# Kernel tuning notes

Measured on AMD Instinct MI355X. Metric: run time of the kernel, lower is better.

The kernel has to match this reference:

```python
import jax, jax.numpy as jnp
import numpy as np

N, F, HID, HEADS, C, E = 4096, 128, 128, 8, 64, 131072
HEAD_DIM = F // HEADS


def gcn_conv(x, row, col, W, b):
    # PyG GCNConv: add self-loops, symmetric normalization, then scatter-add of X@W.
    n = x.shape[0]
    loops = jnp.arange(n)
    r = jnp.concatenate([row, loops])
    c = jnp.concatenate([col, loops])
    deg = jax.ops.segment_sum(jnp.ones_like(c, x.dtype), c, num_segments=n)
    dinv = jnp.where(deg > 0, jax.lax.rsqrt(deg), 0.0)
    norm = dinv[r] * dinv[c]                      # [E+N]
    h = x @ W                                      # [n, out]
    msg = h[r] * norm[:, None]                     # gather + scale
    return jax.ops.segment_sum(msg, c, num_segments=n) + b


def mha(x, in_w, in_b, out_w, out_b):
    # torch nn.MultiheadAttention, unbatched (L, E) self-attention
    n, e = x.shape
    qkv = x @ in_w.T + in_b                        # [n, 3E]
    q, k, v = jnp.split(qkv, 3, axis=-1)
    q = q.reshape(n, HEADS, HEAD_DIM).transpose(1, 0, 2)
    k = k.reshape(n, HEADS, HEAD_DIM).transpose(1, 0, 2)
    v = v.reshape(n, HEADS, HEAD_DIM).transpose(1, 0, 2)
    scores = jnp.einsum('hnd,hmd->hnm', q, k) / jnp.sqrt(jnp.asarray(HEAD_DIM, x.dtype))
    attn = jax.nn.softmax(scores, axis=-1)
    o = jnp.einsum('hnm,hmd->hnd', attn, v).transpose(1, 0, 2).reshape(n, e)
    return o @ out_w.T + out_b


def setup_inputs() -> dict:
    key = jax.random.key(0)
    ks = jax.random.split(key, 14)

    def lin(k, shape, fan_in):
        return jax.random.uniform(k, shape, jnp.float32, -1.0, 1.0) / np.sqrt(fan_in)

    return {
        'x': jax.random.normal(ks[0], (N, F), jnp.float32),
        'edge_index': jax.random.randint(ks[1], (2, E), 0, N),
        'W1': lin(ks[2], (F, HID), F), 'b1': lin(ks[3], (HID,), F),
        'W2': lin(ks[4], (HID, HID), HID), 'b2': lin(ks[5], (HID,), HID),
        'W3': lin(ks[6], (HID, C), HID), 'b3': lin(ks[7], (C,), HID),
        'in_proj_w': lin(ks[8], (3 * F, F), F), 'in_proj_b': jnp.zeros((3 * F,), jnp.float32),
        'out_proj_w': lin(ks[9], (F, F), F), 'out_proj_b': jnp.zeros((F,), jnp.float32),
        'proj_w': lin(ks[10], (F, C), F), 'proj_b': lin(ks[11], (C,), F),
    }


def reference(x, edge_index, W1, b1, W2, b2, W3, b3,
              in_proj_w, in_proj_b, out_proj_w, out_proj_b, proj_w, proj_b):
    row, col = edge_index[0], edge_index[1]
    h = jax.nn.relu(gcn_conv(x, row, col, W1, b1))
    h = jax.nn.relu(gcn_conv(h, row, col, W2, b2))
    x_gnn = h @ W3 + b3                           # [N, C]
    x_tf = mha(x, in_proj_w, in_proj_b, out_proj_w, out_proj_b)
    x_proj = x_tf @ proj_w + proj_b               # [N, C]
    return jax.nn.relu(x_gnn + x_proj)
```

## Files before the change

### kernel.cpp

```cpp
#include <hip/hip_runtime.h>
#include <math.h>

#define N_NODES 4096
#define F_DIM   128
#define E_EDGES 131072
#define NHEADS  8
#define HD      16
#define C_OUT   64

__global__ void deg_count(const int* __restrict__ col, int* __restrict__ deg) {
  int e = blockIdx.x * blockDim.x + threadIdx.x;
  if (e < E_EDGES) atomicAdd(&deg[col[e]], 1);
}

__global__ void dinv_kernel(const int* __restrict__ deg, float* __restrict__ dinv) {
  int i = blockIdx.x * blockDim.x + threadIdx.x;
  if (i < N_NODES) dinv[i] = rsqrtf((float)(deg[i] + 1));
}

__global__ void scan_kernel(const int* __restrict__ deg, int* __restrict__ offs) {
  __shared__ int part[1024];
  int t = threadIdx.x;
  int v0 = deg[t*4+0], v1 = deg[t*4+1], v2 = deg[t*4+2], v3 = deg[t*4+3];
  int s = v0 + v1 + v2 + v3;
  part[t] = s;
  __syncthreads();
  for (int off = 1; off < 1024; off <<= 1) {
    int x = (t >= off) ? part[t - off] : 0;
    __syncthreads();
    part[t] += x;
    __syncthreads();
  }
  int excl = part[t] - s;
  offs[t*4+0] = excl; excl += v0;
  offs[t*4+1] = excl; excl += v1;
  offs[t*4+2] = excl; excl += v2;
  offs[t*4+3] = excl; excl += v3;
  if (t == 1023) offs[4096] = excl;
}

__global__ void fill_csr(const int* __restrict__ row, const int* __restrict__ col,
                         const int* __restrict__ offs, int* __restrict__ cursor,
                         int* __restrict__ src) {
  int e = blockIdx.x * blockDim.x + threadIdx.x;
  if (e < E_EDGES) {
    int c = col[e];
    int p = atomicAdd(&cursor[c], 1);
    src[offs[c] + p] = row[e];
  }
}

__global__ void gcn_agg(const float* __restrict__ t, const float* __restrict__ dinv,
                        const int* __restrict__ offs, const int* __restrict__ src,
                        const float* __restrict__ bias, float* __restrict__ out) {
  int c = blockIdx.x;
  int f = threadIdx.x;
  float dc = dinv[c];
  float acc = t[c * F_DIM + f] * dc;
  int e = offs[c], end = offs[c + 1];
  for (; e + 4 <= end; e += 4) {
    int r0 = src[e], r1 = src[e+1], r2 = src[e+2], r3 = src[e+3];
    float w0 = dinv[r0], w1 = dinv[r1], w2 = dinv[r2], w3 = dinv[r3];
    float v0 = t[r0*F_DIM + f], v1 = t[r1*F_DIM + f];
    float v2 = t[r2*F_DIM + f], v3 = t[r3*F_DIM + f];
    acc += v0*w0 + v1*w1 + v2*w2 + v3*w3;
  }
  for (; e < end; ++e) { int r = src[e]; acc += t[r*F_DIM + f] * dinv[r]; }
  float res = acc * dc + bias[f];
  out[c * F_DIM + f] = fmaxf(res, 0.f);
}

template<int TM, bool NT, bool BIAS, bool RELU, bool EXTRA>
__global__ __launch_bounds__(256) void gemm2(const float* __restrict__ A,
                                             const float* __restrict__ B,
                                             const float* __restrict__ bias,
                                             const float* __restrict__ extra,
                                             float* __restrict__ C,
                                             int ldb, int ldc) {
  constexpr int K = 128, BK = 32, TN = 64;
  constexpr int RM = TM * TN / 1024;
  constexpr int LDA = 36;
  constexpr int LDB = TN + 4;
  __shared__ float As[BK * LDA];
  __shared__ float Bs[BK * LDB];
  const int tid = threadIdx.x;
  const int tx = tid & 15;
  const int ty = tid >> 4;
  const int row0 = blockIdx.x * TM;
  const int jg0  = blockIdx.y * TN;

  float acc[RM][4];
  #pragma unroll
  for (int r = 0; r < RM; ++r) { acc[r][0]=0.f; acc[r][1]=0.f; acc[r][2]=0.f; acc[r][3]=0.f; }

  for (int kc = 0; kc < K; kc += BK) {
    __syncthreads();
    {
      constexpr int NL = TM * BK / 4;
      for (int idx = tid; idx < NL; idx += 256) {
        int m  = idx >> 3;
        int k4 = idx & 7;
        const float4 g = *(const float4*)&A[(row0 + m) * K + kc + k4 * 4];
        As[(k4*4+0)*LDA + m] = g.x;
        As[(k4*4+1)*LDA + m] = g.y;
        As[(k4*4+2)*LDA + m] = g.z;
        As[(k4*4+3)*LDA + m] = g.w;
      }
    }
    if constexpr (NT) {
      constexpr int NL = TN * 8;
      for (int idx = tid; idx < NL; idx += 256) {
        int n  = idx >> 3;
        int k4 = idx & 7;
        const float4 g = *(const float4*)&B[(jg0 + n) * K + kc + k4 * 4];
        Bs[(k4*4+0)*LDB + n] = g.x;
        Bs[(k4*4+1)*LDB + n] = g.y;
        Bs[(k4*4+2)*LDB + n] = g.z;
        Bs[(k4*4+3)*LDB + n] = g.w;
      }
    } else {
      constexpr int NL = BK * TN / 4;
      for (int idx = tid; idx < NL; idx += 256) {
        int k  = idx >> 4;
        int n4 = idx & 15;
        *(float4*)&Bs[k * LDB + n4 * 4] =
            *(const float4*)&B[(kc + k) * ldb + jg0 + n4 * 4];
      }
    }
    __syncthreads();
    #pragma unroll
    for (int k = 0; k < BK; ++k) {
      const float4 bv = *(const float4*)&Bs[k * LDB + tx * 4];
      #pragma unroll
      for (int r = 0; r < RM; ++r) {
        const float a = As[k * LDA + ty * RM + r];
        acc[r][0] = fmaf(a, bv.x, acc[r][0]);
        acc[r][1] = fmaf(a, bv.y, acc[r][1]);
        acc[r][2] = fmaf(a, bv.z, acc[r][2]);
        acc[r][3] = fmaf(a, bv.w, acc[r][3]);
      }
    }
  }

  #pragma unroll
  for (int r = 0; r < RM; ++r) {
    const int gr = row0 + ty * RM + r;
    const int gc = jg0 + tx * 4;
    float4 v = make_float4(acc[r][0], acc[r][1], acc[r][2], acc[r][3]);
    if constexpr (BIAS) {
      const float4 bb = *(const float4*)&bias[gc];
      v.x += bb.x; v.y += bb.y; v.z += bb.z; v.w += bb.w;
    }
    if constexpr (EXTRA) {
      const float4 e = *(const float4*)&extra[gr * ldc + gc];
      v.x += e.x; v.y += e.y; v.z += e.z; v.w += e.w;
    }
    if constexpr (RELU) {
      v.x = fmaxf(v.x, 0.f); v.y = fmaxf(v.y, 0.f);
      v.z = fmaxf(v.z, 0.f); v.w = fmaxf(v.w, 0.f);
    }
    *(float4*)&C[gr * ldc + gc] = v;
  }
}

__global__ __launch_bounds__(256) void attn_kernel(const float* __restrict__ qkv,
                                                   float* __restrict__ o) {
  constexpr int TQ = 64, TK = 512;
  __shared__ float Ks[TK * HD];
  __shared__ float Vs[TK * HD];
  const int h    = blockIdx.y;
  const int rl   = threadIdx.x >> 2;
  const int sub  = threadIdx.x & 3;
  const int rowg = blockIdx.x * TQ + rl;

  const float4* qp = (const float4*)&qkv[rowg * 384 + h * HD];
  float4 q0 = qp[0], q1 = qp[1], q2 = qp[2], q3 = qp[3];
  q0.x*=0.25f; q0.y*=0.25f; q0.z*=0.25f; q0.w*=0.25f;
  q1.x*=0.25f; q1.y*=0.25f; q1.z*=0.25f; q1.w*=0.25f;
  q2.x*=0.25f; q2.y*=0.25f; q2.z*=0.25f; q2.w*=0.25f;
  q3.x*=0.25f; q3.y*=0.25f; q3.z*=0.25f; q3.w*=0.25f;

  float m = -INFINITY, l = 0.f;
  float oa[HD];
  #pragma unroll
  for (int d = 0; d < HD; ++d) oa[d] = 0.f;

  for (int kt = 0; kt < N_NODES; kt += TK) {
    __syncthreads();
    for (int fi = threadIdx.x; fi < TK * HD / 4; fi += 256) {
      int r = fi >> 2, c4 = fi & 3;
      ((float4*)Ks)[fi] = *(const float4*)&qkv[(kt + r) * 384 + 128 + h * HD + c4 * 4];
      ((float4*)Vs)[fi] = *(const float4*)&qkv[(kt + r) * 384 + 256 + h * HD + c4 * 4];
    }
    __syncthreads();

    for (int j0 = 0; j0 < TK; j0 += 32) {
      float s[8];
      #pragma unroll
      for (int i = 0; i < 8; ++i) {
        const float4* kp = (const float4*)&Ks[(j0 + 4*i + sub) * HD];
        const float4 k0 = kp[0], k1 = kp[1], k2 = kp[2], k3 = kp[3];
        float p0 = fmaf(q0.x,k0.x, fmaf(q0.y,k0.y, fmaf(q0.z,k0.z, q0.w*k0.w)));
        float p1 = fmaf(q1.x,k1.x, fmaf(q1.y,k1.y, fmaf(q1.z,k1.z, q1.w*k1.w)));
        float p2 = fmaf(q2.x,k2.x, fmaf(q2.y,k2.y, fmaf(q2.z,k2.z, q2.w*k2.w)));
        float p3 = fmaf(q3.x,k3.x, fmaf(q3.y,k3.y, fmaf(q3.z,k3.z, q3.w*k3.w)));
        s[i] = (p0 + p1) + (p2 + p3);
      }
      float bm = fmaxf(fmaxf(fmaxf(s[0],s[1]), fmaxf(s[2],s[3])),
                       fmaxf(fmaxf(s[4],s[5]), fmaxf(s[6],s[7])));
      float mnew = fmaxf(m, bm);
      float cor = __expf(m - mnew);
      float p[8];
      #pragma unroll
      for (int i = 0; i < 8; ++i) p[i] = __expf(s[i] - mnew);
      float ps = ((p[0]+p[1]) + (p[2]+p[3])) + ((p[4]+p[5]) + (p[6]+p[7]));
      l = fmaf(l, cor, ps);
      m = mnew;
      #pragma unroll
      for (int d = 0; d < HD; ++d) oa[d] *= cor;
      #pragma unroll
      for (int i = 0; i < 8; ++i) {
        const float4* vp = (const float4*)&Vs[(j0 + 4*i + sub) * HD];
        const float4 v0 = vp[0], v1 = vp[1], v2 = vp[2], v3 = vp[3];
        oa[0]  = fmaf(p[i], v0.x, oa[0]);  oa[1]  = fmaf(p[i], v0.y, oa[1]);
        oa[2]  = fmaf(p[i], v0.z, oa[2]);  oa[3]  = fmaf(p[i], v0.w, oa[3]);
        oa[4]  = fmaf(p[i], v1.x, oa[4]);  oa[5]  = fmaf(p[i], v1.y, oa[5]);
        oa[6]  = fmaf(p[i], v1.z, oa[6]);  oa[7]  = fmaf(p[i], v1.w, oa[7]);
        oa[8]  = fmaf(p[i], v2.x, oa[8]);  oa[9]  = fmaf(p[i], v2.y, oa[9]);
        oa[10] = fmaf(p[i], v2.z, oa[10]); oa[11] = fmaf(p[i], v2.w, oa[11]);
        oa[12] = fmaf(p[i], v3.x, oa[12]); oa[13] = fmaf(p[i], v3.y, oa[13]);
        oa[14] = fmaf(p[i], v3.z, oa[14]); oa[15] = fmaf(p[i], v3.w, oa[15]);
      }
    }
  }
  __syncthreads();
  Vs[rl*4 + sub]       = m;
  Vs[256 + rl*4 + sub] = l;
  #pragma unroll
  for (int d = 0; d < HD; ++d) Ks[(rl*4 + sub) * HD + d] = oa[d];
  __syncthreads();
  float m0 = Vs[rl*4+0], m1 = Vs[rl*4+1], m2 = Vs[rl*4+2], m3 = Vs[rl*4+3];
  float M  = fmaxf(fmaxf(m0, m1), fmaxf(m2, m3));
  float w0 = __expf(m0 - M), w1 = __expf(m1 - M), w2 = __expf(m2 - M), w3 = __expf(m3 - M);
  float L  = Vs[256+rl*4+0]*w0 + Vs[256+rl*4+1]*w1 + Vs[256+rl*4+2]*w2 + Vs[256+rl*4+3]*w3;
  float invL = 1.f / L;
  const float* kb = &Ks[rl * 4 * HD];
  int d0 = sub * 4;
  float4 r;
  r.x = (kb[0*HD+d0+0]*w0 + kb[1*HD+d0+0]*w1 + kb[2*HD+d0+0]*w2 + kb[3*HD+d0+0]*w3) * invL;
  r.y = (kb[0*HD+d0+1]*w0 + kb[1*HD+d0+1]*w1 + kb[2*HD+d0+1]*w2 + kb[3*HD+d0+1]*w3) * invL;
  r.z = (kb[0*HD+d0+2]*w0 + kb[1*HD+d0+2]*w1 + kb[2*HD+d0+2]*w2 + kb[3*HD+d0+2]*w3) * invL;
  r.w = (kb[0*HD+d0+3]*w0 + kb[1*HD+d0+3]*w1 + kb[2*HD+d0+3]*w2 + kb[3*HD+d0+3]*w3) * invL;
  *(float4*)&o[rowg * F_DIM + h * HD + d0] = r;
}

extern "C" void kernel_launch(void* const* d_in, const int* in_sizes, int n_in,
                              void* d_out, int out_size, void* d_ws, size_t ws_size,
                              hipStream_t stream) {
  const float* x   = (const float*)d_in[0];
  const int*   ei  = (const int*)  d_in[1];
  const float* W1  = (const float*)d_in[2];
  const float* b1  = (const float*)d_in[3];
  const float* W2  = (const float*)d_in[4];
  const float* b2  = (const float*)d_in[5];
  const float* W3  = (const float*)d_in[6];
  const float* b3  = (const float*)d_in[7];
  const float* ipw = (const float*)d_in[8];
  const float* ipb = (const float*)d_in[9];
  const float* opw = (const float*)d_in[10];
  const float* opb = (const float*)d_in[11];
  const float* pw  = (const float*)d_in[12];
  const float* pb  = (const float*)d_in[13];
  float* out = (float*)d_out;

  int*   deg    = (int*)d_ws;
  int*   cursor = deg + 4096;
  int*   offs   = cursor + 4096;
  int*   csrc   = offs + 4100;
  float* dinv   = (float*)(csrc + E_EDGES);
  float* bufA   = dinv + 4096;
  float* bufB   = bufA + 524288;
  float* qkv    = bufB + 524288;
  float* obuf   = qkv + 1572864;

  const int* rowp = ei;
  const int* colp = ei + E_EDGES;

  hipMemsetAsync(deg, 0, 8192 * sizeof(int), stream);
  deg_count<<<E_EDGES / 256, 256, 0, stream>>>(colp, deg);
  dinv_kernel<<<N_NODES / 256, 256, 0, stream>>>(deg, dinv);
  scan_kernel<<<1, 1024, 0, stream>>>(deg, offs);
  fill_csr<<<E_EDGES / 256, 256, 0, stream>>>(rowp, colp, offs, cursor, csrc);

  gemm2<32, false, false, false, false><<<dim3(128, 2), 256, 0, stream>>>(
      x, W1, nullptr, nullptr, bufA, 128, 128);
  gcn_agg<<<N_NODES, 128, 0, stream>>>(bufA, dinv, offs, csrc, b1, bufB);
  gemm2<32, false, false, false, false><<<dim3(128, 2), 256, 0, stream>>>(
      bufB, W2, nullptr, nullptr, bufA, 128, 128);
  gcn_agg<<<N_NODES, 128, 0, stream>>>(bufA, dinv, offs, csrc, b2, bufB);
  gemm2<16, false, true, false, false><<<dim3(256, 1), 256, 0, stream>>>(
      bufB, W3, b3, nullptr, bufA, 64, C_OUT);

  gemm2<32, true, true, false, false><<<dim3(128, 6), 256, 0, stream>>>(
      x, ipw, ipb, nullptr, qkv, 128, 384);
  attn_kernel<<<dim3(64, NHEADS), 256, 0, stream>>>(qkv, obuf);
  gemm2<32, true, true, false, false><<<dim3(128, 2), 256, 0, stream>>>(
      obuf, opw, opb, nullptr, bufB, 128, 128);
  gemm2<16, false, true, true, true><<<dim3(256, 1), 256, 0, stream>>>(
      bufB, pw, pb, bufA, out, 64, C_OUT);
}
```

Baseline: 382.1 us.

## Fuse dinv into scan, vectorize GCN aggregation, retile attention, merge final GEMMs

Several changes land together. dinv is computed inside the scan kernel, removing one launch. GCN aggregation now gives each node a 32-lane group that loads float4 values, with 8 nodes per block. Attention threads each cover 4 query rows against 16 key slices, for more register reuse per shared-memory load, with a 16-way merge at the end and launch bounds set for 2 blocks. The W3 GEMM and the projection GEMM become one dual-pass GEMM that sums both products with both biases, dropping a kernel and an intermediate write and read. The costs are higher register pressure in attention and a larger final merge step.

Result: faster. 337.2 us (-11.8%).

```diff
diff --git a/kernel.cpp b/kernel.cpp
--- a/kernel.cpp
+++ b/kernel.cpp
@@ -13,15 +13,15 @@
   if (e < E_EDGES) atomicAdd(&deg[col[e]], 1);
 }
 
-__global__ void dinv_kernel(const int* __restrict__ deg, float* __restrict__ dinv) {
-  int i = blockIdx.x * blockDim.x + threadIdx.x;
-  if (i < N_NODES) dinv[i] = rsqrtf((float)(deg[i] + 1));
-}
-
-__global__ void scan_kernel(const int* __restrict__ deg, int* __restrict__ offs) {
+__global__ void scan_kernel(const int* __restrict__ deg, int* __restrict__ offs,
+                            float* __restrict__ dinv) {
   __shared__ int part[1024];
   int t = threadIdx.x;
   int v0 = deg[t*4+0], v1 = deg[t*4+1], v2 = deg[t*4+2], v3 = deg[t*4+3];
+  dinv[t*4+0] = rsqrtf((float)(v0 + 1));
+  dinv[t*4+1] = rsqrtf((float)(v1 + 1));
+  dinv[t*4+2] = rsqrtf((float)(v2 + 1));
+  dinv[t*4+3] = rsqrtf((float)(v3 + 1));
   int s = v0 + v1 + v2 + v3;
   part[t] = s;
   __syncthreads();
@@ -50,31 +50,53 @@
   }
 }
 
-__global__ void gcn_agg(const float* __restrict__ t, const float* __restrict__ dinv,
-                        const int* __restrict__ offs, const int* __restrict__ src,
-                        const float* __restrict__ bias, float* __restrict__ out) {
-  int c = blockIdx.x;
-  int f = threadIdx.x;
-  float dc = dinv[c];
-  float acc = t[c * F_DIM + f] * dc;
-  int e = offs[c], end = offs[c + 1];
-  for (; e + 4 <= end; e += 4) {
-    int r0 = src[e], r1 = src[e+1], r2 = src[e+2], r3 = src[e+3];
-    float w0 = dinv[r0], w1 = dinv[r1], w2 = dinv[r2], w3 = dinv[r3];
-    float v0 = t[r0*F_DIM + f], v1 = t[r1*F_DIM + f];
-    float v2 = t[r2*F_DIM + f], v3 = t[r3*F_DIM + f];
-    acc += v0*w0 + v1*w1 + v2*w2 + v3*w3;
-  }
-  for (; e < end; ++e) { int r = src[e]; acc += t[r*F_DIM + f] * dinv[r]; }
-  float res = acc * dc + bias[f];
-  out[c * F_DIM + f] = fmaxf(res, 0.f);
-}
-
-template<int TM, bool NT, bool BIAS, bool RELU, bool EXTRA>
+__global__ __launch_bounds__(256) void gcn_agg(const float* __restrict__ t,
+                                               const float* __restrict__ dinv,
+                                               const int* __restrict__ offs,
+                                               const int* __restrict__ src,
+                                               const float* __restrict__ bias,
+                                               float* __restrict__ out) {
+  const int node = blockIdx.x * 8 + (threadIdx.x >> 5);
+  const int lane = threadIdx.x & 31;
+  const float dc = dinv[node];
+  float4 a0 = *(const float4*)&t[node * F_DIM + lane * 4];
+  a0.x *= dc; a0.y *= dc; a0.z *= dc; a0.w *= dc;
+  float4 a1 = make_float4(0.f, 0.f, 0.f, 0.f);
+  int e = offs[node], end = offs[node + 1];
+  for (; e + 2 <= end; e += 2) {
+    int r0 = src[e], r1 = src[e + 1];
+    float w0 = dinv[r0], w1 = dinv[r1];
+    const float4 v0 = *(const float4*)&t[r0 * F_DIM + lane * 4];
+    const float4 v1 = *(const float4*)&t[r1 * F_DIM + lane * 4];
+    a0.x = fmaf(w0, v0.x, a0.x); a0.y = fmaf(w0, v0.y, a0.y);
+    a0.z = fmaf(w0, v0.z, a0.z); a0.w = fmaf(w0, v0.w, a0.w);
+    a1.x = fmaf(w1, v1.x, a1.x); a1.y = fmaf(w1, v1.y, a1.y);
+    a1.z = fmaf(w1, v1.z, a1.z); a1.w = fmaf(w1, v1.w, a1.w);
+  }
+  if (e < end) {
+    int r0 = src[e];
+    float w0 = dinv[r0];
+    const float4 v0 = *(const float4*)&t[r0 * F_DIM + lane * 4];
+    a0.x = fmaf(w0, v0.x, a0.x); a0.y = fmaf(w0, v0.y, a0.y);
+    a0.z = fmaf(w0, v0.z, a0.z); a0.w = fmaf(w0, v0.w, a0.w);
+  }
+  a0.x += a1.x; a0.y += a1.y; a0.z += a1.z; a0.w += a1.w;
+  const float4 bb = *(const float4*)&bias[lane * 4];
+  float4 r;
+  r.x = fmaxf(fmaf(a0.x, dc, bb.x), 0.f);
+  r.y = fmaxf(fmaf(a0.y, dc, bb.y), 0.f);
+  r.z = fmaxf(fmaf(a0.z, dc, bb.z), 0.f);
+  r.w = fmaxf(fmaf(a0.w, dc, bb.w), 0.f);
+  *(float4*)&out[node * F_DIM + lane * 4] = r;
+}
+
+template<int TM, bool NT, bool BIAS, bool RELU, bool DUAL>
 __global__ __launch_bounds__(256) void gemm2(const float* __restrict__ A,
                                              const float* __restrict__ B,
                                              const float* __restrict__ bias,
-                                             const float* __restrict__ extra,
+                                             const float* __restrict__ A2,
+                                             const float* __restrict__ B2,
+                                             const float* __restrict__ bias2,
                                              float* __restrict__ C,
                                              int ldb, int ldc) {
   constexpr int K = 128, BK = 32, TN = 64;
@@ -93,51 +115,55 @@
   #pragma unroll
   for (int r = 0; r < RM; ++r) { acc[r][0]=0.f; acc[r][1]=0.f; acc[r][2]=0.f; acc[r][3]=0.f; }
 
-  for (int kc = 0; kc < K; kc += BK) {
-    __syncthreads();
-    {
-      constexpr int NL = TM * BK / 4;
-      for (int idx = tid; idx < NL; idx += 256) {
-        int m  = idx >> 3;
-        int k4 = idx & 7;
-        const float4 g = *(const float4*)&A[(row0 + m) * K + kc + k4 * 4];
-        As[(k4*4+0)*LDA + m] = g.x;
-        As[(k4*4+1)*LDA + m] = g.y;
-        As[(k4*4+2)*LDA + m] = g.z;
-        As[(k4*4+3)*LDA + m] = g.w;
-      }
-    }
-    if constexpr (NT) {
-      constexpr int NL = TN * 8;
-      for (int idx = tid; idx < NL; idx += 256) {
-        int n  = idx >> 3;
-        int k4 = idx & 7;
-        const float4 g = *(const float4*)&B[(jg0 + n) * K + kc + k4 * 4];
-        Bs[(k4*4+0)*LDB + n] = g.x;
-        Bs[(k4*4+1)*LDB + n] = g.y;
-        Bs[(k4*4+2)*LDB + n] = g.z;
-        Bs[(k4*4+3)*LDB + n] = g.w;
-      }
-    } else {
-      constexpr int NL = BK * TN / 4;
-      for (int idx = tid; idx < NL; idx += 256) {
-        int k  = idx >> 4;
-        int n4 = idx & 15;
-        *(float4*)&Bs[k * LDB + n4 * 4] =
-            *(const float4*)&B[(kc + k) * ldb + jg0 + n4 * 4];
-      }
-    }
-    __syncthreads();
-    #pragma unroll
-    for (int k = 0; k < BK; ++k) {
-      const float4 bv = *(const float4*)&Bs[k * LDB + tx * 4];
+  for (int pass = 0; pass < (DUAL ? 2 : 1); ++pass) {
+    const float* Ap = (DUAL && pass) ? A2 : A;
+    const float* Bp = (DUAL && pass) ? B2 : B;
+    for (int kc = 0; kc < K; kc += BK) {
+      __syncthreads();
+      {
+        constexpr int NL = TM * BK / 4;
+        for (int idx = tid; idx < NL; idx += 256) {
+          int m  = idx >> 3;
+          int k4 = idx & 7;
+          const float4 g = *(const float4*)&Ap[(row0 + m) * K + kc + k4 * 4];
+          As[(k4*4+0)*LDA + m] = g.x;
+          As[(k4*4+1)*LDA + m] = g.y;
+          As[(k4*4+2)*LDA + m] = g.z;
+          As[(k4*4+3)*LDA + m] = g.w;
+        }
+      }
+      if constexpr (NT) {
+        constexpr int NL = TN * 8;
+        for (int idx = tid; idx < NL; idx += 256) {
+          int n  = idx >> 3;
+          int k4 = idx & 7;
+          const float4 g = *(const float4*)&Bp[(jg0 + n) * K + kc + k4 * 4];
+          Bs[(k4*4+0)*LDB + n] = g.x;
+          Bs[(k4*4+1)*LDB + n] = g.y;
+          Bs[(k4*4+2)*LDB + n] = g.z;
+          Bs[(k4*4+3)*LDB + n] = g.w;
+        }
+      } else {
+        constexpr int NL = BK * TN / 4;
+        for (int idx = tid; idx < NL; idx += 256) {
+          int k  = idx >> 4;
+          int n4 = idx & 15;
+          *(float4*)&Bs[k * LDB + n4 * 4] =
+              *(const float4*)&Bp[(kc + k) * ldb + jg0 + n4 * 4];
+        }
+      }
+      __syncthreads();
       #pragma unroll
-      for (int r = 0; r < RM; ++r) {
-        const float a = As[k * LDA + ty * RM + r];
-        acc[r][0] = fmaf(a, bv.x, acc[r][0]);
-        acc[r][1] = fmaf(a, bv.y, acc[r][1]);
-        acc[r][2] = fmaf(a, bv.z, acc[r][2]);
-        acc[r][3] = fmaf(a, bv.w, acc[r][3]);
+      for (int k = 0; k < BK; ++k) {
+        const float4 bv = *(const float4*)&Bs[k * LDB + tx * 4];
+        #pragma unroll
+        for (int r = 0; r < RM; ++r) {
+          const float a = As[k * LDA + ty * RM + r];
+          acc[r][0] = fmaf(a, bv.x, acc[r][0]);
+          acc[r][1] = fmaf(a, bv.y, acc[r][1]);
+          acc[r][2] = fmaf(a, bv.z, acc[r][2]);
+          acc[r][3] = fmaf(a, bv.w, acc[r][3]);
+        }
       }
     }
   }
@@ -151,9 +177,9 @@
       const float4 bb = *(const float4*)&bias[gc];
       v.x += bb.x; v.y += bb.y; v.z += bb.z; v.w += bb.w;
     }
-    if constexpr (EXTRA) {
-      const float4 e = *(const float4*)&extra[gr * ldc + gc];
-      v.x += e.x; v.y += e.y; v.z += e.z; v.w += e.w;
+    if constexpr (DUAL) {
+      const float4 bb = *(const float4*)&bias2[gc];
+      v.x += bb.x; v.y += bb.y; v.z += bb.z; v.w += bb.w;
     }
     if constexpr (RELU) {
       v.x = fmaxf(v.x, 0.f); v.y = fmaxf(v.y, 0.f);
@@ -163,27 +189,37 @@
   }
 }
 
-__global__ __launch_bounds__(256) void attn_kernel(const float* __restrict__ qkv,
-                                                   float* __restrict__ o) {
+__global__ __launch_bounds__(256, 2) void attn_kernel(const float* __restrict__ qkv,
+                                                      float* __restrict__ o) {
   constexpr int TQ = 64, TK = 512;
-  __shared__ float Ks[TK * HD];
-  __shared__ float Vs[TK * HD];
-  const int h    = blockIdx.y;
-  const int rl   = threadIdx.x >> 2;
-  const int sub  = threadIdx.x & 3;
-  const int rowg = blockIdx.x * TQ + rl;
-
-  const float4* qp = (const float4*)&qkv[rowg * 384 + h * HD];
-  float4 q0 = qp[0], q1 = qp[1], q2 = qp[2], q3 = qp[3];
-  q0.x*=0.25f; q0.y*=0.25f; q0.z*=0.25f; q0.w*=0.25f;
-  q1.x*=0.25f; q1.y*=0.25f; q1.z*=0.25f; q1.w*=0.25f;
-  q2.x*=0.25f; q2.y*=0.25f; q2.z*=0.25f; q2.w*=0.25f;
-  q3.x*=0.25f; q3.y*=0.25f; q3.z*=0.25f; q3.w*=0.25f;
-
-  float m = -INFINITY, l = 0.f;
-  float oa[HD];
-  #pragma unroll
-  for (int d = 0; d < HD; ++d) oa[d] = 0.f;
+  __shared__ float smem[2 * TK * HD + 2 * TQ * 16];
+  float* Ks = smem;
+  float* Vs = smem + TK * HD;
+  float* mbuf = smem + 2 * TK * HD;
+  float* lbuf = mbuf + TQ * 16;
+  const int h   = blockIdx.y;
+  const int rg  = threadIdx.x >> 4;
+  const int sub = threadIdx.x & 15;
+  const int row0 = blockIdx.x * TQ + rg * 4;
+
+  float4 q[4][4];
+  #pragma unroll
+  for (int r = 0; r < 4; ++r) {
+    const float4* qp = (const float4*)&qkv[(row0 + r) * 384 + h * HD];
+    #pragma unroll
+    for (int c = 0; c < 4; ++c) {
+      float4 v = qp[c];
+      v.x *= 0.25f; v.y *= 0.25f; v.z *= 0.25f; v.w *= 0.25f;
+      q[r][c] = v;
+    }
+  }
+  float m[4] = {-INFINITY, -INFINITY, -INFINITY, -INFINITY};
+  float l[4] = {0.f, 0.f, 0.f, 0.f};
+  float4 oa[4][4];
+  #pragma unroll
+  for (int r = 0; r < 4; ++r)
+    #pragma unroll
+    for (int c = 0; c < 4; ++c) oa[r][c] = make_float4(0.f, 0.f, 0.f, 0.f);
 
   for (int kt = 0; kt < N_NODES; kt += TK) {
     __syncthreads();
@@ -194,64 +230,85 @@
     }
     __syncthreads();
 
-    for (int j0 = 0; j0 < TK; j0 += 32) {
-      float s[8];
+    for (int j0 = 0; j0 < TK; j0 += 64) {
+      float s[4][4];
       #pragma unroll
-      for (int i = 0; i < 8; ++i) {
-        const float4* kp = (const float4*)&Ks[(j0 + 4*i + sub) * HD];
+      for (int kk = 0; kk < 4; ++kk) {
+        const float4* kp = (const float4*)&Ks[(j0 + kk * 16 + sub) * HD];
         const float4 k0 = kp[0], k1 = kp[1], k2 = kp[2], k3 = kp[3];
-        float p0 = fmaf(q0.x,k0.x, fmaf(q0.y,k0.y, fmaf(q0.z,k0.z, q0.w*k0.w)));
-        float p1 = fmaf(q1.x,k1.x, fmaf(q1.y,k1.y, fmaf(q1.z,k1.z, q1.w*k1.w)));
-        float p2 = fmaf(q2.x,k2.x, fmaf(q2.y,k2.y, fmaf(q2.z,k2.z, q2.w*k2.w)));
-        float p3 = fmaf(q3.x,k3.x, fmaf(q3.y,k3.y, fmaf(q3.z,k3.z, q3.w*k3.w)));
-        s[i] = (p0 + p1) + (p2 + p3);
-      }
-      float bm = fmaxf(fmaxf(fmaxf(s[0],s[1]), fmaxf(s[2],s[3])),
-                       fmaxf(fmaxf(s[4],s[5]), fmaxf(s[6],s[7])));
-      float mnew = fmaxf(m, bm);
-      float cor = __expf(m - mnew);
-      float p[8];
+        #pragma unroll
+        for (int r = 0; r < 4; ++r) {
+          float p0 = fmaf(q[r][0].x,k0.x, fmaf(q[r][0].y,k0.y, fmaf(q[r][0].z,k0.z, q[r][0].w*k0.w)));
+          float p1 = fmaf(q[r][1].x,k1.x, fmaf(q[r][1].y,k1.y, fmaf(q[r][1].z,k1.z, q[r][1].w*k1.w)));
+          float p2 = fmaf(q[r][2].x,k2.x, fmaf(q[r][2].y,k2.y, fmaf(q[r][2].z,k2.z, q[r][2].w*k2.w)));
+          float p3 = fmaf(q[r][3].x,k3.x, fmaf(q[r][3].y,k3.y, fmaf(q[r][3].z,k3.z, q[r][3].w*k3.w)));
+          s[r][kk] = (p0 + p1) + (p2 + p3);
+        }
+      }
       #pragma unroll
-      for (int i = 0; i < 8; ++i) p[i] = __expf(s[i] - mnew);
-      float ps = ((p[0]+p[1]) + (p[2]+p[3])) + ((p[4]+p[5]) + (p[6]+p[7]));
-      l = fmaf(l, cor, ps);
-      m = mnew;
+      for (int r = 0; r < 4; ++r) {
+        float bm = fmaxf(fmaxf(s[r][0], s[r][1]), fmaxf(s[r][2], s[r][3]));
+        float mn = fmaxf(m[r], bm);
+        float cor = __expf(m[r] - mn);
+        m[r] = mn;
+        s[r][0] = __expf(s[r][0] - mn);
+        s[r][1] = __expf(s[r][1] - mn);
+        s[r][2] = __expf(s[r][2] - mn);
+        s[r][3] = __expf(s[r][3] - mn);
+        l[r] = fmaf(l[r], cor, (s[r][0] + s[r][1]) + (s[r][2] + s[r][3]));
+        #pragma unroll
+        for (int c = 0; c < 4; ++c) {
+          oa[r][c].x *= cor; oa[r][c].y *= cor; oa[r][c].z *= cor; oa[r][c].w *= cor;
+        }
+      }
       #pragma unroll
-      for (int d = 0; d < HD; ++d) oa[d] *= cor;
-      #pragma unroll
-      for (int i = 0; i < 8; ++i) {
-        const float4* vp = (const float4*)&Vs[(j0 + 4*i + sub) * HD];
+      for (int kk = 0; kk < 4; ++kk) {
+        const float4* vp = (const float4*)&Vs[(j0 + kk * 16 + sub) * HD];
         const float4 v0 = vp[0], v1 = vp[1], v2 = vp[2], v3 = vp[3];
-        oa[0]  = fmaf(p[i], v0.x, oa[0]);  oa[1]  = fmaf(p[i], v0.y, oa[1]);
-        oa[2]  = fmaf(p[i], v0.z, oa[2]);  oa[3]  = fmaf(p[i], v0.w, oa[3]);
-        oa[4]  = fmaf(p[i], v1.x, oa[4]);  oa[5]  = fmaf(p[i], v1.y, oa[5]);
-        oa[6]  = fmaf(p[i], v1.z, oa[6]);  oa[7]  = fmaf(p[i], v1.w, oa[7]);
-        oa[8]  = fmaf(p[i], v2.x, oa[8]);  oa[9]  = fmaf(p[i], v2.y, oa[9]);
-        oa[10] = fmaf(p[i], v2.z, oa[10]); oa[11] = fmaf(p[i], v2.w, oa[11]);
-        oa[12] = fmaf(p[i], v3.x, oa[12]); oa[13] = fmaf(p[i], v3.y, oa[13]);
-        oa[14] = fmaf(p[i], v3.z, oa[14]); oa[15] = fmaf(p[i], v3.w, oa[15]);
+        #pragma unroll
+        for (int r = 0; r < 4; ++r) {
+          const float p = s[r][kk];
+          oa[r][0].x = fmaf(p, v0.x, oa[r][0].x); oa[r][0].y = fmaf(p, v0.y, oa[r][0].y);
+          oa[r][0].z = fmaf(p, v0.z, oa[r][0].z); oa[r][0].w = fmaf(p, v0.w, oa[r][0].w);
+          oa[r][1].x = fmaf(p, v1.x, oa[r][1].x); oa[r][1].y = fmaf(p, v1.y, oa[r][1].y);
+          oa[r][1].z = fmaf(p, v1.z, oa[r][1].z); oa[r][1].w = fmaf(p, v1.w, oa[r][1].w);
+          oa[r][2].x = fmaf(p, v2.x, oa[r][2].x); oa[r][2].y = fmaf(p, v2.y, oa[r][2].y);
+          oa[r][2].z = fmaf(p, v2.z, oa[r][2].z); oa[r][2].w = fmaf(p, v2.w, oa[r][2].w);
+          oa[r][3].x = fmaf(p, v3.x, oa[r][3].x); oa[r][3].y = fmaf(p, v3.y, oa[r][3].y);
+          oa[r][3].z = fmaf(p, v3.z, oa[r][3].z); oa[r][3].w = fmaf(p, v3.w, oa[r][3].w);
+        }
       }
     }
   }
   __syncthreads();
-  Vs[rl*4 + sub]       = m;
-  Vs[256 + rl*4 + sub] = l;
-  #pragma unroll
-  for (int d = 0; d < HD; ++d) Ks[(rl*4 + sub) * HD + d] = oa[d];
+  #pragma unroll
+  for (int r = 0; r < 4; ++r) {
+    const int rl = rg * 4 + r;
+    mbuf[rl * 16 + sub] = m[r];
+    lbuf[rl * 16 + sub] = l[r];
+    #pragma unroll
+    for (int c = 0; c < 4; ++c)
+      *(float4*)&smem[(rl * 16 + sub) * HD + c * 4] = oa[r][c];
+  }
   __syncthreads();
-  float m0 = Vs[rl*4+0], m1 = Vs[rl*4+1], m2 = Vs[rl*4+2], m3 = Vs[rl*4+3];
-  float M  = fmaxf(fmaxf(m0, m1), fmaxf(m2, m3));
-  float w0 = __expf(m0 - M), w1 = __expf(m1 - M), w2 = __expf(m2 - M), w3 = __expf(m3 - M);
-  float L  = Vs[256+rl*4+0]*w0 + Vs[256+rl*4+1]*w1 + Vs[256+rl*4+2]*w2 + Vs[256+rl*4+3]*w3;
-  float invL = 1.f / L;
-  const float* kb = &Ks[rl * 4 * HD];
-  int d0 = sub * 4;
-  float4 r;
-  r.x = (kb[0*HD+d0+0]*w0 + kb[1*HD+d0+0]*w1 + kb[2*HD+d0+0]*w2 + kb[3*HD+d0+0]*w3) * invL;
-  r.y = (kb[0*HD+d0+1]*w0 + kb[1*HD+d0+1]*w1 + kb[2*HD+d0+1]*w2 + kb[3*HD+d0+1]*w3) * invL;
-  r.z = (kb[0*HD+d0+2]*w0 + kb[1*HD+d0+2]*w1 + kb[2*HD+d0+2]*w2 + kb[3*HD+d0+2]*w3) * invL;
-  r.w = (kb[0*HD+d0+3]*w0 + kb[1*HD+d0+3]*w1 + kb[2*HD+d0+3]*w2 + kb[3*HD+d0+3]*w3) * invL;
-  *(float4*)&o[rowg * F_DIM + h * HD + d0] = r;
+  const int row = threadIdx.x >> 2;
+  const int g   = threadIdx.x & 3;
+  float M = -INFINITY;
+  #pragma unroll
+  for (int t16 = 0; t16 < 16; ++t16) M = fmaxf(M, mbuf[row * 16 + t16]);
+  float L = 0.f;
+  float4 acc = make_float4(0.f, 0.f, 0.f, 0.f);
+  #pragma unroll
+  for (int t16 = 0; t16 < 16; ++t16) {
+    const float w = __expf(mbuf[row * 16 + t16] - M);
+    L = fmaf(lbuf[row * 16 + t16], w, L);
+    const float4 ov = *(const float4*)&smem[(row * 16 + t16) * HD + g * 4];
+    acc.x = fmaf(ov.x, w, acc.x); acc.y = fmaf(ov.y, w, acc.y);
+    acc.z = fmaf(ov.z, w, acc.z); acc.w = fmaf(ov.w, w, acc.w);
+  }
+  const float invL = 1.f / L;
+  acc.x *= invL; acc.y *= invL; acc.z *= invL; acc.w *= invL;
+  *(float4*)&o[(blockIdx.x * TQ + row) * F_DIM + h * HD + g * 4] = acc;
 }
 
 extern "C" void kernel_launch(void* const* d_in, const int* in_sizes, int n_in,
@@ -288,24 +345,22 @@
 
   hipMemsetAsync(deg, 0, 8192 * sizeof(int), stream);
   deg_count<<<E_EDGES / 256, 256, 0, stream>>>(colp, deg);
-  dinv_kernel<<<N_NODES / 256, 256, 0, stream>>>(deg, dinv);
-  scan_kernel<<<1, 1024, 0, stream>>>(deg, offs);
+  scan_kernel<<<1, 1024, 0, stream>>>(deg, offs, dinv);
   fill_csr<<<E_EDGES / 256, 256, 0, stream>>>(rowp, colp, offs, cursor, csrc);
 
   gemm2<32, false, false, false, false><<<dim3(128, 2), 256, 0, stream>>>(
-      x, W1, nullptr, nullptr, bufA, 128, 128);
-  gcn_agg<<<N_NODES, 128, 0, stream>>>(bufA, dinv, offs, csrc, b1, bufB);
+      x, W1, nullptr, nullptr, nullptr, nullptr, bufA, 128, 128);
+  gcn_agg<<<N_NODES / 8, 256, 0, stream>>>(bufA, dinv, offs, csrc, b1, bufB);
   gemm2<32, false, false, false, false><<<dim3(128, 2), 256, 0, stream>>>(
-      bufB, W2, nullptr, nullptr, bufA, 128, 128);
-  gcn_agg<<<N_NODES, 128, 0, stream>>>(bufA, dinv, offs, csrc, b2, bufB);
-  gemm2<16, false, true, false, false><<<dim3(256, 1), 256, 0, stream>>>(
-      bufB, W3, b3, nullptr, bufA, 64, C_OUT);
+      bufB, W2, nullptr, nullptr, nullptr, nullptr, bufA, 128, 128);
+  gcn_agg<<<N_NODES / 8, 256, 0, stream>>>(bufA, dinv, offs, csrc, b2, bufB);
 
   gemm2<32, true, true, false, false><<<dim3(128, 6), 256, 0, stream>>>(
-      x, ipw, ipb, nullptr, qkv, 128, 384);
+      x, ipw, ipb, nullptr, nullptr, nullptr, qkv, 128, 384);
   attn_kernel<<<dim3(64, NHEADS), 256, 0, stream>>>(qkv, obuf);
   gemm2<32, true, true, false, false><<<dim3(128, 2), 256, 0, stream>>>(
-      obuf, opw, opb, nullptr, bufB, 128, 128);
+      obuf, opw, opb, nullptr, nullptr, nullptr, bufA, 128, 128);
+
   gemm2<16, false, true, true, true><<<dim3(256, 1), 256, 0, stream>>>(
-      bufB, pw, pb, bufA, out, 64, C_OUT);
-}
+      bufB, W3, b3, bufA, pw, pb, out, 64, C_OUT);
+}
```
